# Kernel tuning notes

Measured on AMD Instinct MI355X. Metric: run time of the kernel, lower is better.

Reference implementation:

```python
import jax, jax.numpy as jnp
import numpy as np

B = 256      # batch size (molecules)
A = 64       # num_atoms per molecule
N = B * A    # total nodes = 16384
E = 262144   # num edges
H = 128      # hidden_dim
L = 4        # num_layers
LAT = 64     # latent_dim
AF = 16      # atom_feature_dim
LN_EPS = 1e-5


def setup_inputs() -> dict:
    key = jax.random.key(0)
    ks = jax.random.split(key, 26)
    w = lambda k, shape: (jax.random.normal(k, shape) * 0.05).astype(jnp.float32)
    inp = {}
    inp["z"] = jax.random.normal(ks[0], (B, LAT), jnp.float32)
    inp["atom_types"] = jax.nn.one_hot(
        jax.random.randint(ks[1], (N,), 0, AF), AF, dtype=jnp.float32)
    inp["pos0"] = jax.random.normal(ks[2], (N, 3), jnp.float32) * 0.1
    inp["edge_index"] = jax.random.randint(ks[3], (2, E), 0, N)
    # latent injector: Linear(LAT+AF, 2H) -> SiLU -> Linear(2H, H) -> SiLU -> Linear(H, H)
    inp["inj_W1"] = w(ks[4], (AF + LAT, 2 * H)); inp["inj_b1"] = jnp.zeros((2 * H,), jnp.float32)
    inp["inj_W2"] = w(ks[5], (2 * H, H));        inp["inj_b2"] = jnp.zeros((H,), jnp.float32)
    inp["inj_W3"] = w(ks[6], (H, H));            inp["inj_b3"] = jnp.zeros((H,), jnp.float32)
    # per-layer params, stacked over layer dim L
    inp["edge_W1"] = w(ks[7], (L, 2 * H + 1, H)); inp["edge_b1"] = jnp.zeros((L, H), jnp.float32)
    inp["edge_W2"] = w(ks[8], (L, H, H));         inp["edge_b2"] = jnp.zeros((L, H), jnp.float32)
    inp["coord_W1"] = w(ks[9], (L, H, H));        inp["coord_b1"] = jnp.zeros((L, H), jnp.float32)
    inp["coord_W2"] = w(ks[10], (L, H, 1))  # no bias
    inp["node_W1"] = w(ks[11], (L, 2 * H, H));    inp["node_b1"] = jnp.zeros((L, H), jnp.float32)
    inp["node_W2"] = w(ks[12], (L, H, H));        inp["node_b2"] = jnp.zeros((L, H), jnp.float32)
    inp["ln_g"] = jnp.ones((L, H), jnp.float32)
    inp["ln_b"] = jnp.zeros((L, H), jnp.float32)
    return inp


def _layer_norm(x, g, b):
    mu = jnp.mean(x, axis=-1, keepdims=True)
    var = jnp.mean((x - mu) ** 2, axis=-1, keepdims=True)
    return (x - mu) * jax.lax.rsqrt(var + LN_EPS) * g + b


def _egnn_layer(h, pos, row, col, eW1, eb1, eW2, eb2, cW1, cb1, cW2, nW1, nb1, nW2, nb2, g, b):
    # --- message: gather endpoints, edge MLP ---
    rel = pos[row] - pos[col]                                   # [E, 3]
    dsq = jnp.clip(jnp.sum(rel * rel, axis=1, keepdims=True), 1e-6, 1e6)  # [E, 1]
    ef = jnp.concatenate([h[row], h[col], dsq], axis=1)         # [E, 2H+1]
    m = jax.nn.silu(ef @ eW1 + eb1)
    m = jax.nn.silu(m @ eW2 + eb2)
    m = jnp.clip(m, -10.0, 10.0)                                # [E, H]
    # --- coordinate update: coord MLP -> weighted rel_pos -> scatter_add, mean-normalized ---
    cw = jax.nn.silu(m @ cW1 + cb1) @ cW2                       # [E, 1]
    coord_update = jax.ops.segment_sum(cw * rel, row, num_segments=N)   # [N, 3]
    num_neighbors = jax.ops.segment_sum(jnp.ones((row.shape[0],), m.dtype), row, num_segments=N)[:, None]
    pos_new = pos + coord_update / (num_neighbors + 1e-6)
    # --- node update: scatter_add messages, node MLP, residual + LayerNorm ---
    agg = jax.ops.segment_sum(m, row, num_segments=N)           # [N, H]
    nu = jnp.concatenate([h, agg], axis=1)                      # [N, 2H]
    nu = jax.nn.silu(nu @ nW1 + nb1) @ nW2 + nb2
    h_new = _layer_norm(h + nu, g, b)
    return h_new, pos_new


def reference(z, atom_types, pos0, edge_index,
              inj_W1, inj_b1, inj_W2, inj_b2, inj_W3, inj_b3,
              edge_W1, edge_b1, edge_W2, edge_b2,
              coord_W1, coord_b1, coord_W2,
              node_W1, node_b1, node_W2, node_b2,
              ln_g, ln_b):
    # latent injection: h = MLP(cat[atom_types, repeat_interleave(z, num_atoms)])
    z_exp = jnp.repeat(z, A, axis=0)                            # [N, LAT]
    h = jnp.concatenate([atom_types, z_exp], axis=1)            # [N, AF+LAT]
    h = jax.nn.silu(h @ inj_W1 + inj_b1)
    h = jax.nn.silu(h @ inj_W2 + inj_b2)
    h = h @ inj_W3 + inj_b3                                     # [N, H]
    pos = pos0
    row, col = edge_index[0], edge_index[1]
    for l in range(L):
        h, pos = _egnn_layer(h, pos, row, col,
                             edge_W1[l], edge_b1[l], edge_W2[l], edge_b2[l],
                             coord_W1[l], coord_b1[l], coord_W2[l],
                             node_W1[l], node_b1[l], node_W2[l], node_b2[l],
                             ln_g[l], ln_b[l])
    return pos
```

## Files before the change

### kernel.cpp

```cpp
#include <hip/hip_runtime.h>
#include <cmath>

#define N_NODES 16384
#define E_EDGES 262144
#define HD 128
#define NLAYER 4

typedef __attribute__((ext_vector_type(8))) short bf16x8;
typedef __attribute__((ext_vector_type(4))) float f32x4;
#define MFMA16(a, b, c) __builtin_amdgcn_mfma_f32_16x16x32_bf16(a, b, c, 0, 0, 0)

__device__ __forceinline__ float silu_f(float x) {
  return __fdividef(x, 1.0f + __expf(-x));
}

__device__ __forceinline__ unsigned short bf16_rn(float f) {
  union { float f; unsigned u; } v; v.f = f;
  unsigned r = (v.u + 0x7FFFu + ((v.u >> 16) & 1u)) >> 16;
  return (unsigned short)r;
}
__device__ __forceinline__ float bf16_tof(unsigned short h) {
  union { unsigned u; float f; } v; v.u = ((unsigned)h) << 16; return v.f;
}

__global__ void k_prep_w(const float* __restrict__ eW1, const float* __restrict__ eW2,
                         const float* __restrict__ cW1,
                         unsigned short* __restrict__ e1f, unsigned short* __restrict__ e2f,
                         unsigned short* __restrict__ c1f) {
  int sid = blockIdx.x * 256 + threadIdx.x;
  int layer = sid >> 13;
  int r = sid & 8191;
  const float* src; unsigned short* base; int c, s, halfstride;
  if (r < 4096) {
    c = r >> 9; s = r & 511;
    src = eW1 + (size_t)layer * 257 * 128;
    base = e1f + (size_t)layer * 65536; halfstride = 32768;
  } else if (r < 6144) {
    int rr = r - 4096; c = rr >> 9; s = rr & 511;
    src = eW2 + (size_t)layer * 128 * 128;
    base = e2f + (size_t)layer * 32768; halfstride = 16384;
  } else {
    int rr = r - 6144; c = rr >> 9; s = rr & 511;
    src = cW1 + (size_t)layer * 128 * 128;
    base = c1f + (size_t)layer * 32768; halfstride = 16384;
  }
  int cf = s >> 6, lp = s & 63;
  int n = cf * 16 + (lp & 15);
  int k0 = c * 32 + (lp >> 4) * 8;
  bf16x8 hv, lv;
#pragma unroll
  for (int j = 0; j < 8; ++j) {
    float w = src[(size_t)(k0 + j) * 128 + n];
    unsigned short h = bf16_rn(w);
    hv[j] = (short)h;
    lv[j] = (short)bf16_rn(w - bf16_tof(h));
  }
  size_t off = ((size_t)c * 512 + s) * 8;
  *(bf16x8*)(base + off) = hv;
  *(bf16x8*)(base + halfstride + off) = lv;
}

__global__ void k_h2bf(const float* __restrict__ h, unsigned short* __restrict__ hhi,
                       unsigned short* __restrict__ hlo) {
  int i = (blockIdx.x * 256 + threadIdx.x) * 8;
  float4 a = *(const float4*)(h + i), b = *(const float4*)(h + i + 4);
  float v[8] = {a.x, a.y, a.z, a.w, b.x, b.y, b.z, b.w};
  bf16x8 hv, lv;
#pragma unroll
  for (int j = 0; j < 8; ++j) {
    unsigned u = __float_as_uint(v[j]);
    hv[j] = (short)(u >> 16);
    float hi_f = __uint_as_float(u & 0xFFFF0000u);
    lv[j] = (short)bf16_rn(v[j] - hi_f);
  }
  *(bf16x8*)(hhi + i) = hv;
  *(bf16x8*)(hlo + i) = lv;
}

__global__ __launch_bounds__(256, 3) void k_edge_mfma(
    const unsigned short* __restrict__ hhi, const unsigned short* __restrict__ hlo,
    const float* __restrict__ pos,
    const int* __restrict__ rows, const int* __restrict__ cols, const int* __restrict__ perm,
    const unsigned short* __restrict__ e1f, const float* __restrict__ eW1,
    const float* __restrict__ eb1,
    const unsigned short* __restrict__ e2f, const float* __restrict__ eb2,
    const unsigned short* __restrict__ c1f, const float* __restrict__ cb1,
    const float* __restrict__ cW2,
    float* __restrict__ agg, float* __restrict__ coordacc) {
  __shared__ __align__(16) float T[64][132];
  __shared__ __align__(16) short Bl[2][4096];
  __shared__ int srow[64], scol[64];
  __shared__ float sdsq[64];
  __shared__ float srel[64][4];

  const int tid = threadIdx.x;
  const int lane = tid & 63;
  const int w = tid >> 6;
  const int l15 = lane & 15, l4 = lane >> 4;
  const int j0 = blockIdx.x * 64;
  const f32x4 zero4 = {0.f, 0.f, 0.f, 0.f};

  if (tid < 64) {
    int e = perm[j0 + tid];
    int r = rows[e], c = cols[e];
    srow[tid] = r; scol[tid] = c;
    float rx = pos[r * 3 + 0] - pos[c * 3 + 0];
    float ry = pos[r * 3 + 1] - pos[c * 3 + 1];
    float rz = pos[r * 3 + 2] - pos[c * 3 + 2];
    srel[tid][0] = rx; srel[tid][1] = ry; srel[tid][2] = rz;
    float d = rx * rx + ry * ry + rz * rz;
    sdsq[tid] = fminf(fmaxf(d, 1e-6f), 1e6f);
  }

  f32x4 acc[8];

#pragma unroll
  for (int i = 0; i < 8; ++i) acc[i] = zero4;
  for (int c = 0; c < 8; ++c) {
    __syncthreads();
#pragma unroll
    for (int t = 0; t < 4; ++t) {
      int slot = tid + t * 256;
      int half = slot >> 9, rem = slot & 511;
      const unsigned short* src = e1f + (size_t)half * 32768 + ((size_t)c * 512 + rem) * 8;
      *(bf16x8*)(&Bl[half][rem * 8]) = *(const bf16x8*)src;
    }
    __syncthreads();
    int node = (c < 4 ? srow : scol)[16 * w + l15];
    int koff = (c & 3) * 32 + l4 * 8;
    bf16x8 ah = *(const bf16x8*)(hhi + (size_t)node * 128 + koff);
    bf16x8 al = *(const bf16x8*)(hlo + (size_t)node * 128 + koff);
#pragma unroll
    for (int cf = 0; cf < 8; ++cf) {
      bf16x8 bh = *(const bf16x8*)(&Bl[0][cf * 512 + lane * 8]);
      bf16x8 bl = *(const bf16x8*)(&Bl[1][cf * 512 + lane * 8]);
      acc[cf] = MFMA16(ah, bh, acc[cf]);
      acc[cf] = MFMA16(al, bh, acc[cf]);
      acc[cf] = MFMA16(ah, bl, acc[cf]);
    }
  }
#pragma unroll
  for (int cf = 0; cf < 8; ++cf) {
    int col = cf * 16 + l15;
    float wl = eW1[256 * 128 + col];
    float bb = eb1[col];
#pragma unroll
    for (int r = 0; r < 4; ++r) {
      int trow = 16 * w + l4 * 4 + r;
      T[trow][col] = silu_f(acc[cf][r] + sdsq[trow] * wl + bb);
    }
  }

#pragma unroll
  for (int i = 0; i < 8; ++i) acc[i] = zero4;
  for (int c = 0; c < 4; ++c) {
    __syncthreads();
#pragma unroll
    for (int t = 0; t < 4; ++t) {
      int slot = tid + t * 256;
      int half = slot >> 9, rem = slot & 511;
      const unsigned short* src = e2f + (size_t)half * 16384 + ((size_t)c * 512 + rem) * 8;
      *(bf16x8*)(&Bl[half][rem * 8]) = *(const bf16x8*)src;
    }
    __syncthreads();
    int trow = 16 * w + l15;
    int k0 = c * 32 + l4 * 8;
    float tv[8];
    *(float4*)(tv) = *(const float4*)(&T[trow][k0]);
    *(float4*)(tv + 4) = *(const float4*)(&T[trow][k0 + 4]);
    bf16x8 ah, al;
#pragma unroll
    for (int j = 0; j < 8; ++j) {
      unsigned u = __float_as_uint(tv[j]);
      ah[j] = (short)(u >> 16);
      float hi_f = __uint_as_float(u & 0xFFFF0000u);
      al[j] = (short)bf16_rn(tv[j] - hi_f);
    }
#pragma unroll
    for (int cf = 0; cf < 8; ++cf) {
      bf16x8 bh = *(const bf16x8*)(&Bl[0][cf * 512 + lane * 8]);
      bf16x8 bl = *(const bf16x8*)(&Bl[1][cf * 512 + lane * 8]);
      acc[cf] = MFMA16(ah, bh, acc[cf]);
      acc[cf] = MFMA16(al, bh, acc[cf]);
      acc[cf] = MFMA16(ah, bl, acc[cf]);
    }
  }
#pragma unroll
  for (int cf = 0; cf < 8; ++cf) {
    int col = cf * 16 + l15;
    float bb = eb2[col];
#pragma unroll
    for (int r = 0; r < 4; ++r) {
      int trow = 16 * w + l4 * 4 + r;
      float v = silu_f(acc[cf][r] + bb);
      v = fminf(fmaxf(v, -10.0f), 10.0f);
      acc[cf][r] = v;
      T[trow][col] = v;
    }
  }
  {
    int seg = 0;
    while (seg < 16) {
      int node = srow[16 * w + seg];
      int se = seg + 1;
      while (se < 16 && srow[16 * w + se] == node) ++se;
#pragma unroll
      for (int cf = 0; cf < 8; ++cf) {
        float s = 0.f;
#pragma unroll
        for (int r = 0; r < 4; ++r) {
          int row = l4 * 4 + r;
          s += (row >= seg && row < se) ? acc[cf][r] : 0.f;
        }
        s += __shfl_xor(s, 16);
        s += __shfl_xor(s, 32);
        if (l4 == 0) atomicAdd(&agg[(size_t)node * 128 + cf * 16 + l15], s);
      }
      seg = se;
    }
  }

#pragma unroll
  for (int i = 0; i < 8; ++i) acc[i] = zero4;
  for (int c = 0; c < 4; ++c) {
    __syncthreads();
#pragma unroll
    for (int t = 0; t < 4; ++t) {
      int slot = tid + t * 256;
      int half = slot >> 9, rem = slot & 511;
      const unsigned short* src = c1f + (size_t)half * 16384 + ((size_t)c * 512 + rem) * 8;
      *(bf16x8*)(&Bl[half][rem * 8]) = *(const bf16x8*)src;
    }
    __syncthreads();
    int trow = 16 * w + l15;
    int k0 = c * 32 + l4 * 8;
    float tv[8];
    *(float4*)(tv) = *(const float4*)(&T[trow][k0]);
    *(float4*)(tv + 4) = *(const float4*)(&T[trow][k0 + 4]);
    bf16x8 ah, al;
#pragma unroll
    for (int j = 0; j < 8; ++j) {
      unsigned u = __float_as_uint(tv[j]);
      ah[j] = (short)(u >> 16);
      float hi_f = __uint_as_float(u & 0xFFFF0000u);
      al[j] = (short)bf16_rn(tv[j] - hi_f);
    }
#pragma unroll
    for (int cf = 0; cf < 8; ++cf) {
      bf16x8 bh = *(const bf16x8*)(&Bl[0][cf * 512 + lane * 8]);
      bf16x8 bl = *(const bf16x8*)(&Bl[1][cf * 512 + lane * 8]);
      acc[cf] = MFMA16(ah, bh, acc[cf]);
      acc[cf] = MFMA16(al, bh, acc[cf]);
      acc[cf] = MFMA16(ah, bl, acc[cf]);
    }
  }
  {
    float p[4] = {0.f, 0.f, 0.f, 0.f};
#pragma unroll
    for (int cf = 0; cf < 8; ++cf) {
      int col = cf * 16 + l15;
      float bb = cb1[col];
      float w2 = cW2[col];
#pragma unroll
      for (int r = 0; r < 4; ++r) p[r] += silu_f(acc[cf][r] + bb) * w2;
    }
#pragma unroll
    for (int d = 1; d < 16; d <<= 1) {
#pragma unroll
      for (int r = 0; r < 4; ++r) p[r] += __shfl_xor(p[r], d);
    }
    int seg = 0;
    while (seg < 16) {
      int node = srow[16 * w + seg];
      int se = seg + 1;
      while (se < 16 && srow[16 * w + se] == node) ++se;
      float s = 0.f;
      if (l15 < 3) {
#pragma unroll
        for (int r = 0; r < 4; ++r) {
          int row = l4 * 4 + r;
          s += (row >= seg && row < se) ? p[r] * srel[16 * w + row][l15] : 0.f;
        }
      }
      s += __shfl_xor(s, 16);
      s += __shfl_xor(s, 32);
      if (l4 == 0 && l15 < 3) atomicAdd(&coordacc[(size_t)node * 4 + l15], s);
      seg = se;
    }
  }
}

__global__ void k_pos_fin(const float* __restrict__ coordacc, const int* __restrict__ offs,
                          float* __restrict__ pos) {
  int n = blockIdx.x * 256 + threadIdx.x;
  if (n < N_NODES) {
    float deg = (float)(offs[n + 1] - offs[n]);
    float inv = __fdividef(1.0f, deg + 1e-6f);
    pos[n * 3 + 0] += coordacc[n * 4 + 0] * inv;
    pos[n * 3 + 1] += coordacc[n * 4 + 1] * inv;
    pos[n * 3 + 2] += coordacc[n * 4 + 2] * inv;
  }
}

template <int ACT>
__global__ __launch_bounds__(256, 2) void k_gemm128(const float* Ag, const float* __restrict__ W,
                                                    const float* __restrict__ bias, float* C, int K) {
  __shared__ float As[64][33];
  __shared__ float Ws[32][128];
  const int tid = threadIdx.x;
  const int tc = tid & 15, tr = tid >> 4;
  const int tr4 = tr * 4, tc4 = tc * 4;
  const int m0 = blockIdx.x * 64;

  float acc[4][8];
#pragma unroll
  for (int i = 0; i < 4; ++i)
#pragma unroll
    for (int j = 0; j < 8; ++j) acc[i][j] = 0.0f;

  for (int kk = 0; kk < K; kk += 32) {
    int idx = tid;
#pragma unroll
    for (int it = 0; it < 2; ++it, idx += 256) {
      int r = idx >> 3, c4 = (idx & 7) << 2;
      float4 v = *(const float4*)(Ag + (size_t)(m0 + r) * K + kk + c4);
      As[r][c4] = v.x; As[r][c4 + 1] = v.y; As[r][c4 + 2] = v.z; As[r][c4 + 3] = v.w;
    }
    idx = tid;
#pragma unroll
    for (int it = 0; it < 4; ++it, idx += 256) {
      int r = idx >> 5, c4 = (idx & 31) << 2;
      *(float4*)(&Ws[r][c4]) = *(const float4*)(W + (size_t)(kk + r) * 128 + c4);
    }
    __syncthreads();
#pragma unroll
    for (int k = 0; k < 32; ++k) {
      float av[4];
#pragma unroll
      for (int i = 0; i < 4; ++i) av[i] = As[tr4 + i][k];
      float4 b0 = *(const float4*)(&Ws[k][tc4]);
      float4 b1 = *(const float4*)(&Ws[k][64 + tc4]);
      float bv[8] = {b0.x, b0.y, b0.z, b0.w, b1.x, b1.y, b1.z, b1.w};
#pragma unroll
      for (int i = 0; i < 4; ++i)
#pragma unroll
        for (int j = 0; j < 8; ++j) acc[i][j] = fmaf(av[i], bv[j], acc[i][j]);
    }
    __syncthreads();
  }

  float bv0[8];
#pragma unroll
  for (int j = 0; j < 4; ++j) { bv0[j] = bias[tc4 + j]; bv0[4 + j] = bias[64 + tc4 + j]; }
#pragma unroll
  for (int i = 0; i < 4; ++i) {
    size_t row = m0 + tr4 + i;
    float o[8];
#pragma unroll
    for (int j = 0; j < 8; ++j) {
      float v = acc[i][j] + bv0[j];
      if (ACT >= 1) v = silu_f(v);
      o[j] = v;
    }
    *(float4*)(C + row * 128 + tc4) = make_float4(o[0], o[1], o[2], o[3]);
    *(float4*)(C + row * 128 + 64 + tc4) = make_float4(o[4], o[5], o[6], o[7]);
  }
}

__global__ void k_count(const int* __restrict__ rows, int* __restrict__ cnt) {
  int e = blockIdx.x * 256 + threadIdx.x;
  if (e < E_EDGES) atomicAdd(&cnt[rows[e]], 1);
}

__global__ void k_scan(const int* __restrict__ cnt, int* __restrict__ offs) {
  __shared__ int part[256];
  const int tid = threadIdx.x;
  const int base = tid * 64;
  int s = 0;
  for (int i = 0; i < 64; ++i) s += cnt[base + i];
  part[tid] = s;
  __syncthreads();
  for (int d = 1; d < 256; d <<= 1) {
    int v = (tid >= d) ? part[tid - d] : 0;
    __syncthreads();
    part[tid] += v;
    __syncthreads();
  }
  int run = part[tid] - s;
  for (int i = 0; i < 64; ++i) { offs[base + i] = run; run += cnt[base + i]; }
  if (tid == 255) offs[N_NODES] = run;
}

__global__ void k_fill(const int* __restrict__ rows, const int* __restrict__ offs,
                       int* __restrict__ fill, int* __restrict__ perm) {
  int e = blockIdx.x * 256 + threadIdx.x;
  if (e < E_EDGES) {
    int r = rows[e];
    int p = atomicAdd(&fill[r], 1);
    perm[offs[r] + p] = e;
  }
}

__global__ __launch_bounds__(256, 2) void k_node_mlp(float* __restrict__ h, const float* __restrict__ agg,
                                                     const float* __restrict__ W1, const float* __restrict__ b1,
                                                     const float* __restrict__ W2, const float* __restrict__ b2,
                                                     const float* __restrict__ lng, const float* __restrict__ lnb) {
  __shared__ float As[64][33];
  __shared__ float Ws[32][128];
  __shared__ float T[64][132];
  const int tid = threadIdx.x;
  const int tc = tid & 15, tr = tid >> 4;
  const int tr4 = tr * 4, tc4 = tc * 4;
  const int m0 = blockIdx.x * 64;

  float acc[4][8];
#pragma unroll
  for (int i = 0; i < 4; ++i)
#pragma unroll
    for (int j = 0; j < 8; ++j) acc[i][j] = 0.0f;

  for (int kk = 0; kk < 256; kk += 32) {
    const float* src = (kk < 128) ? h : agg;
    const int kb = kk & 127;
    int idx = tid;
#pragma unroll
    for (int it = 0; it < 2; ++it, idx += 256) {
      int r = idx >> 3, c4 = (idx & 7) << 2;
      float4 v = *(const float4*)(src + (size_t)(m0 + r) * 128 + kb + c4);
      As[r][c4] = v.x; As[r][c4 + 1] = v.y; As[r][c4 + 2] = v.z; As[r][c4 + 3] = v.w;
    }
    idx = tid;
#pragma unroll
    for (int it = 0; it < 4; ++it, idx += 256) {
      int r = idx >> 5, c4 = (idx & 31) << 2;
      *(float4*)(&Ws[r][c4]) = *(const float4*)(W1 + (size_t)(kk + r) * 128 + c4);
    }
    __syncthreads();
#pragma unroll
    for (int k = 0; k < 32; ++k) {
      float av[4];
#pragma unroll
      for (int i = 0; i < 4; ++i) av[i] = As[tr4 + i][k];
      float4 b0 = *(const float4*)(&Ws[k][tc4]);
      float4 b1v = *(const float4*)(&Ws[k][64 + tc4]);
      float bv[8] = {b0.x, b0.y, b0.z, b0.w, b1v.x, b1v.y, b1v.z, b1v.w};
#pragma unroll
      for (int i = 0; i < 4; ++i)
#pragma unroll
        for (int j = 0; j < 8; ++j) acc[i][j] = fmaf(av[i], bv[j], acc[i][j]);
    }
    __syncthreads();
  }
#pragma unroll
  for (int i = 0; i < 4; ++i) {
#pragma unroll
    for (int j = 0; j < 4; ++j) {
      T[tr4 + i][tc4 + j] = silu_f(acc[i][j] + b1[tc4 + j]);
      T[tr4 + i][64 + tc4 + j] = silu_f(acc[i][4 + j] + b1[64 + tc4 + j]);
    }
  }
  __syncthreads();

  float acc2[4][8];
#pragma unroll
  for (int i = 0; i < 4; ++i)
#pragma unroll
    for (int j = 0; j < 8; ++j) acc2[i][j] = 0.0f;
  for (int kk = 0; kk < 128; kk += 32) {
    int idx = tid;
#pragma unroll
    for (int it = 0; it < 4; ++it, idx += 256) {
      int r = idx >> 5, c4 = (idx & 31) << 2;
      *(float4*)(&Ws[r][c4]) = *(const float4*)(W2 + (size_t)(kk + r) * 128 + c4);
    }
    __syncthreads();
#pragma unroll
    for (int k = 0; k < 32; ++k) {
      float av[4];
#pragma unroll
      for (int i = 0; i < 4; ++i) av[i] = T[tr4 + i][kk + k];
      float4 b0 = *(const float4*)(&Ws[k][tc4]);
      float4 b1v = *(const float4*)(&Ws[k][64 + tc4]);
      float bv[8] = {b0.x, b0.y, b0.z, b0.w, b1v.x, b1v.y, b1v.z, b1v.w};
#pragma unroll
      for (int i = 0; i < 4; ++i)
#pragma unroll
        for (int j = 0; j < 8; ++j) acc2[i][j] = fmaf(av[i], bv[j], acc2[i][j]);
    }
    __syncthreads();
  }

  float x[4][8], s1[4], s2[4];
#pragma unroll
  for (int i = 0; i < 4; ++i) {
    size_t row = m0 + tr4 + i;
    float4 h0 = *(const float4*)(h + row * 128 + tc4);
    float4 h1 = *(const float4*)(h + row * 128 + 64 + tc4);
    float hv[8] = {h0.x, h0.y, h0.z, h0.w, h1.x, h1.y, h1.z, h1.w};
    s1[i] = 0.f; s2[i] = 0.f;
#pragma unroll
    for (int j = 0; j < 8; ++j) {
      int cidx = (j < 4) ? (tc4 + j) : (64 + tc4 + (j - 4));
      float v = hv[j] + acc2[i][j] + b2[cidx];
      x[i][j] = v;
      s1[i] += v;
      s2[i] += v * v;
    }
  }
#pragma unroll
  for (int d = 1; d < 16; d <<= 1) {
#pragma unroll
    for (int i = 0; i < 4; ++i) {
      s1[i] += __shfl_xor(s1[i], d);
      s2[i] += __shfl_xor(s2[i], d);
    }
  }
  float gv[8], bvv[8];
#pragma unroll
  for (int j = 0; j < 4; ++j) {
    gv[j] = lng[tc4 + j]; gv[4 + j] = lng[64 + tc4 + j];
    bvv[j] = lnb[tc4 + j]; bvv[4 + j] = lnb[64 + tc4 + j];
  }
#pragma unroll
  for (int i = 0; i < 4; ++i) {
    float mu = s1[i] * (1.0f / 128.0f);
    float var = s2[i] * (1.0f / 128.0f) - mu * mu;
    float rs = rsqrtf(var + 1e-5f);
    size_t row = m0 + tr4 + i;
    float o[8];
#pragma unroll
    for (int j = 0; j < 8; ++j) o[j] = (x[i][j] - mu) * rs * gv[j] + bvv[j];
    *(float4*)(h + row * 128 + tc4) = make_float4(o[0], o[1], o[2], o[3]);
    *(float4*)(h + row * 128 + 64 + tc4) = make_float4(o[4], o[5], o[6], o[7]);
  }
}

__global__ __launch_bounds__(256) void k_inj1(const float* __restrict__ at, const float* __restrict__ z,
                                              const float* __restrict__ W1, const float* __restrict__ b1,
                                              float* __restrict__ out) {
  __shared__ float As[64][84];
  __shared__ float Ws[80][128];
  const int tid = threadIdx.x;
  const int tc = tid & 15, tr = tid >> 4;
  const int tr4 = tr * 4, tc4 = tc * 4;
  const int m0 = blockIdx.y * 64;
  const int cb = blockIdx.x * 128;

  int idx = tid;
#pragma unroll
  for (int it = 0; it < 5; ++it, idx += 256) {
    int r = idx / 20, c4 = idx % 20;
    int n = m0 + r;
    float4 v;
    if (c4 < 4) v = *(const float4*)(at + (size_t)n * 16 + c4 * 4);
    else v = *(const float4*)(z + (size_t)(n >> 6) * 64 + (c4 - 4) * 4);
    *(float4*)(&As[r][c4 * 4]) = v;
  }
  idx = tid;
#pragma unroll
  for (int it = 0; it < 10; ++it, idx += 256) {
    int r = idx >> 5, c4 = (idx & 31) << 2;
    *(float4*)(&Ws[r][c4]) = *(const float4*)(W1 + (size_t)r * 256 + cb + c4);
  }
  __syncthreads();

  float acc[4][8];
#pragma unroll
  for (int i = 0; i < 4; ++i)
#pragma unroll
    for (int j = 0; j < 8; ++j) acc[i][j] = 0.0f;
#pragma unroll 4
  for (int k = 0; k < 80; ++k) {
    float av[4];
#pragma unroll
    for (int i = 0; i < 4; ++i) av[i] = As[tr4 + i][k];
    float4 b0 = *(const float4*)(&Ws[k][tc4]);
    float4 b1v = *(const float4*)(&Ws[k][64 + tc4]);
    float bv[8] = {b0.x, b0.y, b0.z, b0.w, b1v.x, b1v.y, b1v.z, b1v.w};
#pragma unroll
    for (int i = 0; i < 4; ++i)
#pragma unroll
      for (int j = 0; j < 8; ++j) acc[i][j] = fmaf(av[i], bv[j], acc[i][j]);
  }

  float bb[8];
#pragma unroll
  for (int j = 0; j < 4; ++j) { bb[j] = b1[cb + tc4 + j]; bb[4 + j] = b1[cb + 64 + tc4 + j]; }
#pragma unroll
  for (int i = 0; i < 4; ++i) {
    size_t row = m0 + tr4 + i;
    float o[8];
#pragma unroll
    for (int j = 0; j < 8; ++j) o[j] = silu_f(acc[i][j] + bb[j]);
    *(float4*)(out + row * 256 + cb + tc4) = make_float4(o[0], o[1], o[2], o[3]);
    *(float4*)(out + row * 256 + cb + 64 + tc4) = make_float4(o[4], o[5], o[6], o[7]);
  }
}

__global__ void k_copyf(const float* __restrict__ in, float* __restrict__ out, int n) {
  int i = blockIdx.x * 256 + threadIdx.x;
  if (i < n) out[i] = in[i];
}

extern "C" void kernel_launch(void* const* d_in, const int* in_sizes, int n_in,
                              void* d_out, int out_size, void* d_ws, size_t ws_size,
                              hipStream_t stream) {
  const float* z = (const float*)d_in[0];
  const float* at = (const float*)d_in[1];
  const float* pos0 = (const float*)d_in[2];
  const int* ei = (const int*)d_in[3];
  const float* injW1 = (const float*)d_in[4];
  const float* injb1 = (const float*)d_in[5];
  const float* injW2 = (const float*)d_in[6];
  const float* injb2 = (const float*)d_in[7];
  const float* injW3 = (const float*)d_in[8];
  const float* injb3 = (const float*)d_in[9];
  const float* eW1 = (const float*)d_in[10];
  const float* eb1 = (const float*)d_in[11];
  const float* eW2 = (const float*)d_in[12];
  const float* eb2 = (const float*)d_in[13];
  const float* cW1 = (const float*)d_in[14];
  const float* cb1 = (const float*)d_in[15];
  const float* cW2 = (const float*)d_in[16];
  const float* nW1 = (const float*)d_in[17];
  const float* nb1 = (const float*)d_in[18];
  const float* nW2 = (const float*)d_in[19];
  const float* nb2 = (const float*)d_in[20];
  const float* lng = (const float*)d_in[21];
  const float* lnb = (const float*)d_in[22];

  float* w = (float*)d_ws;
  float* h = w;        w += (size_t)N_NODES * HD;
  float* pos = w;      w += (size_t)N_NODES * 3;
  float* agg = w;      w += (size_t)N_NODES * HD;
  float* coordacc = w; w += (size_t)N_NODES * 4;
  float* t1 = w;       w += (size_t)N_NODES * 256;
  float* t2 = w;       w += (size_t)N_NODES * HD;
  unsigned short* hhi = (unsigned short*)w;
  unsigned short* hlo = hhi + (size_t)N_NODES * HD;
  unsigned short* e1f = hlo + (size_t)N_NODES * HD;
  unsigned short* e2f = e1f + (size_t)4 * 65536;
  unsigned short* c1f = e2f + (size_t)4 * 32768;
  int* ib = (int*)(c1f + (size_t)4 * 32768);
  int* cnt = ib;  ib += N_NODES;
  int* offs = ib; ib += N_NODES + 1;
  int* fill = ib; ib += N_NODES;
  int* perm = ib; ib += E_EDGES;

  const int* rowsp = ei;
  const int* colsp = ei + E_EDGES;

  hipMemsetAsync(cnt, 0, N_NODES * sizeof(int), stream);
  hipMemsetAsync(fill, 0, N_NODES * sizeof(int), stream);
  k_count<<<E_EDGES / 256, 256, 0, stream>>>(rowsp, cnt);
  k_scan<<<1, 256, 0, stream>>>(cnt, offs);
  k_fill<<<E_EDGES / 256, 256, 0, stream>>>(rowsp, offs, fill, perm);
  k_copyf<<<(N_NODES * 3 + 255) / 256, 256, 0, stream>>>(pos0, pos, N_NODES * 3);

  k_prep_w<<<128, 256, 0, stream>>>(eW1, eW2, cW1, e1f, e2f, c1f);

  k_inj1<<<dim3(2, N_NODES / 64), 256, 0, stream>>>(at, z, injW1, injb1, t1);
  k_gemm128<1><<<N_NODES / 64, 256, 0, stream>>>(t1, injW2, injb2, t2, 256);
  k_gemm128<0><<<N_NODES / 64, 256, 0, stream>>>(t2, injW3, injb3, h, 128);

  for (int l = 0; l < NLAYER; ++l) {
    hipMemsetAsync(agg, 0, (size_t)N_NODES * HD * sizeof(float), stream);
    hipMemsetAsync(coordacc, 0, (size_t)N_NODES * 4 * sizeof(float), stream);
    k_h2bf<<<(N_NODES * HD / 8) / 256, 256, 0, stream>>>(h, hhi, hlo);
    k_edge_mfma<<<E_EDGES / 64, 256, 0, stream>>>(
        hhi, hlo, pos, rowsp, colsp, perm,
        e1f + (size_t)l * 65536, eW1 + (size_t)l * 257 * HD, eb1 + l * HD,
        e2f + (size_t)l * 32768, eb2 + l * HD,
        c1f + (size_t)l * 32768, cb1 + l * HD,
        cW2 + (size_t)l * HD,
        agg, coordacc);
    k_pos_fin<<<N_NODES / 256, 256, 0, stream>>>(coordacc, offs, pos);
    k_node_mlp<<<N_NODES / 64, 256, 0, stream>>>(h, agg, nW1 + (size_t)l * 2 * HD * HD, nb1 + l * HD,
                                                 nW2 + (size_t)l * HD * HD, nb2 + l * HD,
                                                 lng + l * HD, lnb + l * HD);
  }
  k_copyf<<<(N_NODES * 3 + 255) / 256, 256, 0, stream>>>(pos, (float*)d_out, N_NODES * 3);
}
```

Measured before the change: 1.088 ms.

## Repartition edge MFMA warps by column tiles and store split-bf16 intermediates

```diff
diff --git a/kernel.cpp b/kernel.cpp
--- a/kernel.cpp
+++ b/kernel.cpp
@@ -87,7 +87,8 @@
     const unsigned short* __restrict__ c1f, const float* __restrict__ cb1,
     const float* __restrict__ cW2,
     float* __restrict__ agg, float* __restrict__ coordacc) {
-  __shared__ __align__(16) float T[64][132];
+  __shared__ __align__(16) unsigned short Thi[64][136];
+  __shared__ __align__(16) unsigned short Tlo[64][136];
   __shared__ __align__(16) short Bl[2][4096];
   __shared__ int srow[64], scol[64];
   __shared__ float sdsq[64];
@@ -112,10 +113,10 @@
     sdsq[tid] = fminf(fmaxf(d, 1e-6f), 1e6f);
   }
 
-  f32x4 acc[8];
-
-#pragma unroll
-  for (int i = 0; i < 8; ++i) acc[i] = zero4;
+  f32x4 acc[4][2];
+
+#pragma unroll
+  for (int rt = 0; rt < 4; ++rt) { acc[rt][0] = zero4; acc[rt][1] = zero4; }
   for (int c = 0; c < 8; ++c) {
     __syncthreads();
 #pragma unroll
@@ -126,33 +127,47 @@
       *(bf16x8*)(&Bl[half][rem * 8]) = *(const bf16x8*)src;
     }
     __syncthreads();
-    int node = (c < 4 ? srow : scol)[16 * w + l15];
+    bf16x8 bh[2], bl[2];
+#pragma unroll
+    for (int cfl = 0; cfl < 2; ++cfl) {
+      int cf = 2 * w + cfl;
+      bh[cfl] = *(const bf16x8*)(&Bl[0][cf * 512 + lane * 8]);
+      bl[cfl] = *(const bf16x8*)(&Bl[1][cf * 512 + lane * 8]);
+    }
+    const int* nodes = (c < 4) ? srow : scol;
     int koff = (c & 3) * 32 + l4 * 8;
-    bf16x8 ah = *(const bf16x8*)(hhi + (size_t)node * 128 + koff);
-    bf16x8 al = *(const bf16x8*)(hlo + (size_t)node * 128 + koff);
-#pragma unroll
-    for (int cf = 0; cf < 8; ++cf) {
-      bf16x8 bh = *(const bf16x8*)(&Bl[0][cf * 512 + lane * 8]);
-      bf16x8 bl = *(const bf16x8*)(&Bl[1][cf * 512 + lane * 8]);
-      acc[cf] = MFMA16(ah, bh, acc[cf]);
-      acc[cf] = MFMA16(al, bh, acc[cf]);
-      acc[cf] = MFMA16(ah, bl, acc[cf]);
-    }
-  }
-#pragma unroll
-  for (int cf = 0; cf < 8; ++cf) {
-    int col = cf * 16 + l15;
+#pragma unroll
+    for (int rt = 0; rt < 4; ++rt) {
+      int node = nodes[rt * 16 + l15];
+      bf16x8 ah = *(const bf16x8*)(hhi + (size_t)node * 128 + koff);
+      bf16x8 al = *(const bf16x8*)(hlo + (size_t)node * 128 + koff);
+#pragma unroll
+      for (int cfl = 0; cfl < 2; ++cfl) {
+        acc[rt][cfl] = MFMA16(ah, bh[cfl], acc[rt][cfl]);
+        acc[rt][cfl] = MFMA16(al, bh[cfl], acc[rt][cfl]);
+        acc[rt][cfl] = MFMA16(ah, bl[cfl], acc[rt][cfl]);
+      }
+    }
+  }
+#pragma unroll
+  for (int cfl = 0; cfl < 2; ++cfl) {
+    int col = (2 * w + cfl) * 16 + l15;
     float wl = eW1[256 * 128 + col];
     float bb = eb1[col];
 #pragma unroll
-    for (int r = 0; r < 4; ++r) {
-      int trow = 16 * w + l4 * 4 + r;
-      T[trow][col] = silu_f(acc[cf][r] + sdsq[trow] * wl + bb);
-    }
-  }
-
-#pragma unroll
-  for (int i = 0; i < 8; ++i) acc[i] = zero4;
+    for (int rt = 0; rt < 4; ++rt)
+#pragma unroll
+      for (int r = 0; r < 4; ++r) {
+        int trow = rt * 16 + l4 * 4 + r;
+        float v = silu_f(acc[rt][cfl][r] + sdsq[trow] * wl + bb);
+        unsigned u = __float_as_uint(v);
+        Thi[trow][col] = (unsigned short)(u >> 16);
+        Tlo[trow][col] = bf16_rn(v - __uint_as_float(u & 0xFFFF0000u));
+      }
+  }
+
+#pragma unroll
+  for (int rt = 0; rt < 4; ++rt) { acc[rt][0] = zero4; acc[rt][1] = zero4; }
   for (int c = 0; c < 4; ++c) {
     __syncthreads();
 #pragma unroll
@@ -163,65 +178,73 @@
       *(bf16x8*)(&Bl[half][rem * 8]) = *(const bf16x8*)src;
     }
     __syncthreads();
-    int trow = 16 * w + l15;
+    bf16x8 bh[2], bl[2];
+#pragma unroll
+    for (int cfl = 0; cfl < 2; ++cfl) {
+      int cf = 2 * w + cfl;
+      bh[cfl] = *(const bf16x8*)(&Bl[0][cf * 512 + lane * 8]);
+      bl[cfl] = *(const bf16x8*)(&Bl[1][cf * 512 + lane * 8]);
+    }
     int k0 = c * 32 + l4 * 8;
-    float tv[8];
-    *(float4*)(tv) = *(const float4*)(&T[trow][k0]);
-    *(float4*)(tv + 4) = *(const float4*)(&T[trow][k0 + 4]);
-    bf16x8 ah, al;
-#pragma unroll
-    for (int j = 0; j < 8; ++j) {
-      unsigned u = __float_as_uint(tv[j]);
-      ah[j] = (short)(u >> 16);
-      float hi_f = __uint_as_float(u & 0xFFFF0000u);
-      al[j] = (short)bf16_rn(tv[j] - hi_f);
-    }
-#pragma unroll
-    for (int cf = 0; cf < 8; ++cf) {
-      bf16x8 bh = *(const bf16x8*)(&Bl[0][cf * 512 + lane * 8]);
-      bf16x8 bl = *(const bf16x8*)(&Bl[1][cf * 512 + lane * 8]);
-      acc[cf] = MFMA16(ah, bh, acc[cf]);
-      acc[cf] = MFMA16(al, bh, acc[cf]);
-      acc[cf] = MFMA16(ah, bl, acc[cf]);
-    }
-  }
-#pragma unroll
-  for (int cf = 0; cf < 8; ++cf) {
-    int col = cf * 16 + l15;
+#pragma unroll
+    for (int rt = 0; rt < 4; ++rt) {
+      int trow = rt * 16 + l15;
+      bf16x8 ah = *(const bf16x8*)(&Thi[trow][k0]);
+      bf16x8 al = *(const bf16x8*)(&Tlo[trow][k0]);
+#pragma unroll
+      for (int cfl = 0; cfl < 2; ++cfl) {
+        acc[rt][cfl] = MFMA16(ah, bh[cfl], acc[rt][cfl]);
+        acc[rt][cfl] = MFMA16(al, bh[cfl], acc[rt][cfl]);
+        acc[rt][cfl] = MFMA16(ah, bl[cfl], acc[rt][cfl]);
+      }
+    }
+  }
+  __syncthreads();
+#pragma unroll
+  for (int cfl = 0; cfl < 2; ++cfl) {
+    int col = (2 * w + cfl) * 16 + l15;
     float bb = eb2[col];
 #pragma unroll
-    for (int r = 0; r < 4; ++r) {
-      int trow = 16 * w + l4 * 4 + r;
-      float v = silu_f(acc[cf][r] + bb);
-      v = fminf(fmaxf(v, -10.0f), 10.0f);
-      acc[cf][r] = v;
-      T[trow][col] = v;
-    }
+    for (int rt = 0; rt < 4; ++rt)
+#pragma unroll
+      for (int r = 0; r < 4; ++r) {
+        int trow = rt * 16 + l4 * 4 + r;
+        float v = silu_f(acc[rt][cfl][r] + bb);
+        v = fminf(fmaxf(v, -10.0f), 10.0f);
+        acc[rt][cfl][r] = v;
+        unsigned u = __float_as_uint(v);
+        Thi[trow][col] = (unsigned short)(u >> 16);
+        Tlo[trow][col] = bf16_rn(v - __uint_as_float(u & 0xFFFF0000u));
+      }
   }
   {
     int seg = 0;
-    while (seg < 16) {
-      int node = srow[16 * w + seg];
+    while (seg < 64) {
+      int node = srow[seg];
       int se = seg + 1;
-      while (se < 16 && srow[16 * w + se] == node) ++se;
-#pragma unroll
-      for (int cf = 0; cf < 8; ++cf) {
+      while (se < 64 && srow[se] == node) ++se;
+#pragma unroll
+      for (int cfl = 0; cfl < 2; ++cfl) {
         float s = 0.f;
 #pragma unroll
-        for (int r = 0; r < 4; ++r) {
-          int row = l4 * 4 + r;
-          s += (row >= seg && row < se) ? acc[cf][r] : 0.f;
+        for (int rt = 0; rt < 4; ++rt) {
+          if (rt * 16 + 15 < seg || rt * 16 >= se) continue;
+#pragma unroll
+          for (int r = 0; r < 4; ++r) {
+            int row = rt * 16 + l4 * 4 + r;
+            s += (row >= seg && row < se) ? acc[rt][cfl][r] : 0.f;
+          }
         }
         s += __shfl_xor(s, 16);
         s += __shfl_xor(s, 32);
-        if (l4 == 0) atomicAdd(&agg[(size_t)node * 128 + cf * 16 + l15], s);
+        if (l4 == 0) atomicAdd(&agg[(size_t)node * 128 + (2 * w + cfl) * 16 + l15], s);
       }
       seg = se;
     }
   }
 
 #pragma unroll
-  for (int i = 0; i < 8; ++i) acc[i] = zero4;
+  for (int rt = 0; rt < 4; ++rt) { acc[rt][0] = zero4; acc[rt][1] = zero4; }
   for (int c = 0; c < 4; ++c) {
     __syncthreads();
 #pragma unroll
@@ -232,54 +255,65 @@
       *(bf16x8*)(&Bl[half][rem * 8]) = *(const bf16x8*)src;
     }
     __syncthreads();
-    int trow = 16 * w + l15;
+    bf16x8 bh[2], bl[2];
+#pragma unroll
+    for (int cfl = 0; cfl < 2; ++cfl) {
+      int cf = 2 * w + cfl;
+      bh[cfl] = *(const bf16x8*)(&Bl[0][cf * 512 + lane * 8]);
+      bl[cfl] = *(const bf16x8*)(&Bl[1][cf * 512 + lane * 8]);
+    }
     int k0 = c * 32 + l4 * 8;
-    float tv[8];
-    *(float4*)(tv) = *(const float4*)(&T[trow][k0]);
-    *(float4*)(tv + 4) = *(const float4*)(&T[trow][k0 + 4]);
-    bf16x8 ah, al;
-#pragma unroll
-    for (int j = 0; j < 8; ++j) {
-      unsigned u = __float_as_uint(tv[j]);
-      ah[j] = (short)(u >> 16);
-      float hi_f = __uint_as_float(u & 0xFFFF0000u);
-      al[j] = (short)bf16_rn(tv[j] - hi_f);
-    }
-#pragma unroll
-    for (int cf = 0; cf < 8; ++cf) {
-      bf16x8 bh = *(const bf16x8*)(&Bl[0][cf * 512 + lane * 8]);
-      bf16x8 bl = *(const bf16x8*)(&Bl[1][cf * 512 + lane * 8]);
-      acc[cf] = MFMA16(ah, bh, acc[cf]);
-      acc[cf] = MFMA16(al, bh, acc[cf]);
-      acc[cf] = MFMA16(ah, bl, acc[cf]);
+#pragma unroll
+    for (int rt = 0; rt < 4; ++rt) {
+      int trow = rt * 16 + l15;
+      bf16x8 ah = *(const bf16x8*)(&Thi[trow][k0]);
+      bf16x8 al = *(const bf16x8*)(&Tlo[trow][k0]);
+#pragma unroll
+      for (int cfl = 0; cfl < 2; ++cfl) {
+        acc[rt][cfl] = MFMA16(ah, bh[cfl], acc[rt][cfl]);
+        acc[rt][cfl] = MFMA16(al, bh[cfl], acc[rt][cfl]);
+        acc[rt][cfl] = MFMA16(ah, bl[cfl], acc[rt][cfl]);
+      }
     }
   }
   {
-    float p[4] = {0.f, 0.f, 0.f, 0.f};
-#pragma unroll
-    for (int cf = 0; cf < 8; ++cf) {
-      int col = cf * 16 + l15;
+    float p[4][4];
+#pragma unroll
+    for (int rt = 0; rt < 4; ++rt)
+#pragma unroll
+      for (int r = 0; r < 4; ++r) p[rt][r] = 0.f;
+#pragma unroll
+    for (int cfl = 0; cfl < 2; ++cfl) {
+      int col = (2 * w + cfl) * 16 + l15;
       float bb = cb1[col];
       float w2 = cW2[col];
 #pragma unroll
-      for (int r = 0; r < 4; ++r) p[r] += silu_f(acc[cf][r] + bb) * w2;
+      for (int rt = 0; rt < 4; ++rt)
+#pragma unroll
+        for (int r = 0; r < 4; ++r) p[rt][r] += silu_f(acc[rt][cfl][r] + bb) * w2;
     }
 #pragma unroll
     for (int d = 1; d < 16; d <<= 1) {
 #pragma unroll
-      for (int r = 0; r < 4; ++r) p[r] += __shfl_xor(p[r], d);
+      for (int rt = 0; rt < 4; ++rt)
+#pragma unroll
+        for (int r = 0; r < 4; ++r) p[rt][r] += __shfl_xor(p[rt][r], d);
     }
     int seg = 0;
-    while (seg < 16) {
-      int node = srow[16 * w + seg];
+    while (seg < 64) {
+      int node = srow[seg];
       int se = seg + 1;
-      while (se < 16 && srow[16 * w + se] == node) ++se;
+      while (se < 64 && srow[se] == node) ++se;
       float s = 0.f;
       if (l15 < 3) {
 #pragma unroll
-        for (int r = 0; r < 4; ++r) {
-          int row = l4 * 4 + r;
-          s += (row >= seg && row < se) ? p[r] * srel[16 * w + row][l15] : 0.f;
+        for (int rt = 0; rt < 4; ++rt) {
+          if (rt * 16 + 15 < seg || rt * 16 >= se) continue;
+#pragma unroll
+          for (int r = 0; r < 4; ++r) {
+            int row = rt * 16 + l4 * 4 + r;
+            s += (row >= seg && row < se) ? p[rt][r] * srel[row][l15] : 0.f;
+          }
         }
       }
       s += __shfl_xor(s, 16);
@@ -404,7 +438,9 @@
 __global__ __launch_bounds__(256, 2) void k_node_mlp(float* __restrict__ h, const float* __restrict__ agg,
                                                      const float* __restrict__ W1, const float* __restrict__ b1,
                                                      const float* __restrict__ W2, const float* __restrict__ b2,
-                                                     const float* __restrict__ lng, const float* __restrict__ lnb) {
+                                                     const float* __restrict__ lng, const float* __restrict__ lnb,
+                                                     unsigned short* __restrict__ hhi,
+                                                     unsigned short* __restrict__ hlo) {
   __shared__ float As[64][33];
   __shared__ float Ws[32][128];
   __shared__ float T[64][132];
@@ -528,10 +564,24 @@
     float rs = rsqrtf(var + 1e-5f);
     size_t row = m0 + tr4 + i;
     float o[8];
-#pragma unroll
-    for (int j = 0; j < 8; ++j) o[j] = (x[i][j] - mu) * rs * gv[j] + bvv[j];
+    unsigned hv16[8], lv16[8];
+#pragma unroll
+    for (int j = 0; j < 8; ++j) {
+      o[j] = (x[i][j] - mu) * rs * gv[j] + bvv[j];
+      unsigned u = __float_as_uint(o[j]);
+      hv16[j] = u >> 16;
+      lv16[j] = bf16_rn(o[j] - __uint_as_float(u & 0xFFFF0000u));
+    }
     *(float4*)(h + row * 128 + tc4) = make_float4(o[0], o[1], o[2], o[3]);
     *(float4*)(h + row * 128 + 64 + tc4) = make_float4(o[4], o[5], o[6], o[7]);
+    *(uint2*)(hhi + row * 128 + tc4) =
+        make_uint2(hv16[0] | (hv16[1] << 16), hv16[2] | (hv16[3] << 16));
+    *(uint2*)(hhi + row * 128 + 64 + tc4) =
+        make_uint2(hv16[4] | (hv16[5] << 16), hv16[6] | (hv16[7] << 16));
+    *(uint2*)(hlo + row * 128 + tc4) =
+        make_uint2(lv16[0] | (lv16[1] << 16), lv16[2] | (lv16[3] << 16));
+    *(uint2*)(hlo + row * 128 + 64 + tc4) =
+        make_uint2(lv16[4] | (lv16[5] << 16), lv16[6] | (lv16[7] << 16));
   }
 }
 
@@ -662,11 +712,11 @@
   k_inj1<<<dim3(2, N_NODES / 64), 256, 0, stream>>>(at, z, injW1, injb1, t1);
   k_gemm128<1><<<N_NODES / 64, 256, 0, stream>>>(t1, injW2, injb2, t2, 256);
   k_gemm128<0><<<N_NODES / 64, 256, 0, stream>>>(t2, injW3, injb3, h, 128);
+  k_h2bf<<<(N_NODES * HD / 8) / 256, 256, 0, stream>>>(h, hhi, hlo);
 
   for (int l = 0; l < NLAYER; ++l) {
     hipMemsetAsync(agg, 0, (size_t)N_NODES * HD * sizeof(float), stream);
     hipMemsetAsync(coordacc, 0, (size_t)N_NODES * 4 * sizeof(float), stream);
-    k_h2bf<<<(N_NODES * HD / 8) / 256, 256, 0, stream>>>(h, hhi, hlo);
     k_edge_mfma<<<E_EDGES / 64, 256, 0, stream>>>(
         hhi, hlo, pos, rowsp, colsp, perm,
         e1f + (size_t)l * 65536, eW1 + (size_t)l * 257 * HD, eb1 + l * HD,
@@ -677,7 +727,7 @@
     k_pos_fin<<<N_NODES / 256, 256, 0, stream>>>(coordacc, offs, pos);
     k_node_mlp<<<N_NODES / 64, 256, 0, stream>>>(h, agg, nW1 + (size_t)l * 2 * HD * HD, nb1 + l * HD,
                                                  nW2 + (size_t)l * HD * HD, nb2 + l * HD,
-                                                 lng + l * HD, lnb + l * HD);
+                                                 lng + l * HD, lnb + l * HD, hhi, hlo);
   }
   k_copyf<<<(N_NODES * 3 + 255) / 256, 256, 0, stream>>>(pos, (float*)d_out, N_NODES * 3);
 }
```

Result: slower. 1.364 ms (+25.4%).

## Load MFMA weight fragments from global directly and fuse bf16 split into node MLP

Applied to the files above, without the earlier changes.

```diff
diff --git a/kernel.cpp b/kernel.cpp
--- a/kernel.cpp
+++ b/kernel.cpp
@@ -77,7 +77,7 @@
   *(bf16x8*)(hlo + i) = lv;
 }
 
-__global__ __launch_bounds__(256, 3) void k_edge_mfma(
+__global__ __launch_bounds__(256, 4) void k_edge_mfma(
     const unsigned short* __restrict__ hhi, const unsigned short* __restrict__ hlo,
     const float* __restrict__ pos,
     const int* __restrict__ rows, const int* __restrict__ cols, const int* __restrict__ perm,
@@ -88,7 +88,6 @@
     const float* __restrict__ cW2,
     float* __restrict__ agg, float* __restrict__ coordacc) {
   __shared__ __align__(16) float T[64][132];
-  __shared__ __align__(16) short Bl[2][4096];
   __shared__ int srow[64], scol[64];
   __shared__ float sdsq[64];
   __shared__ float srel[64][4];
@@ -111,29 +110,22 @@
     float d = rx * rx + ry * ry + rz * rz;
     sdsq[tid] = fminf(fmaxf(d, 1e-6f), 1e6f);
   }
+  __syncthreads();
 
   f32x4 acc[8];
 
 #pragma unroll
   for (int i = 0; i < 8; ++i) acc[i] = zero4;
   for (int c = 0; c < 8; ++c) {
-    __syncthreads();
-#pragma unroll
-    for (int t = 0; t < 4; ++t) {
-      int slot = tid + t * 256;
-      int half = slot >> 9, rem = slot & 511;
-      const unsigned short* src = e1f + (size_t)half * 32768 + ((size_t)c * 512 + rem) * 8;
-      *(bf16x8*)(&Bl[half][rem * 8]) = *(const bf16x8*)src;
-    }
-    __syncthreads();
     int node = (c < 4 ? srow : scol)[16 * w + l15];
     int koff = (c & 3) * 32 + l4 * 8;
     bf16x8 ah = *(const bf16x8*)(hhi + (size_t)node * 128 + koff);
     bf16x8 al = *(const bf16x8*)(hlo + (size_t)node * 128 + koff);
+    const unsigned short* b0 = e1f + (size_t)c * 4096 + (size_t)lane * 8;
 #pragma unroll
     for (int cf = 0; cf < 8; ++cf) {
-      bf16x8 bh = *(const bf16x8*)(&Bl[0][cf * 512 + lane * 8]);
-      bf16x8 bl = *(const bf16x8*)(&Bl[1][cf * 512 + lane * 8]);
+      bf16x8 bh = *(const bf16x8*)(b0 + cf * 512);
+      bf16x8 bl = *(const bf16x8*)(b0 + 32768 + cf * 512);
       acc[cf] = MFMA16(ah, bh, acc[cf]);
       acc[cf] = MFMA16(al, bh, acc[cf]);
       acc[cf] = MFMA16(ah, bl, acc[cf]);
@@ -154,15 +146,6 @@
 #pragma unroll
   for (int i = 0; i < 8; ++i) acc[i] = zero4;
   for (int c = 0; c < 4; ++c) {
-    __syncthreads();
-#pragma unroll
-    for (int t = 0; t < 4; ++t) {
-      int slot = tid + t * 256;
-      int half = slot >> 9, rem = slot & 511;
-      const unsigned short* src = e2f + (size_t)half * 16384 + ((size_t)c * 512 + rem) * 8;
-      *(bf16x8*)(&Bl[half][rem * 8]) = *(const bf16x8*)src;
-    }
-    __syncthreads();
     int trow = 16 * w + l15;
     int k0 = c * 32 + l4 * 8;
     float tv[8];
@@ -176,10 +159,11 @@
       float hi_f = __uint_as_float(u & 0xFFFF0000u);
       al[j] = (short)bf16_rn(tv[j] - hi_f);
     }
+    const unsigned short* b0 = e2f + (size_t)c * 4096 + (size_t)lane * 8;
 #pragma unroll
     for (int cf = 0; cf < 8; ++cf) {
-      bf16x8 bh = *(const bf16x8*)(&Bl[0][cf * 512 + lane * 8]);
-      bf16x8 bl = *(const bf16x8*)(&Bl[1][cf * 512 + lane * 8]);
+      bf16x8 bh = *(const bf16x8*)(b0 + cf * 512);
+      bf16x8 bl = *(const bf16x8*)(b0 + 16384 + cf * 512);
       acc[cf] = MFMA16(ah, bh, acc[cf]);
       acc[cf] = MFMA16(al, bh, acc[cf]);
       acc[cf] = MFMA16(ah, bl, acc[cf]);
@@ -223,15 +207,6 @@
 #pragma unroll
   for (int i = 0; i < 8; ++i) acc[i] = zero4;
   for (int c = 0; c < 4; ++c) {
-    __syncthreads();
-#pragma unroll
-    for (int t = 0; t < 4; ++t) {
-      int slot = tid + t * 256;
-      int half = slot >> 9, rem = slot & 511;
-      const unsigned short* src = c1f + (size_t)half * 16384 + ((size_t)c * 512 + rem) * 8;
-      *(bf16x8*)(&Bl[half][rem * 8]) = *(const bf16x8*)src;
-    }
-    __syncthreads();
     int trow = 16 * w + l15;
     int k0 = c * 32 + l4 * 8;
     float tv[8];
@@ -245,10 +220,11 @@
       float hi_f = __uint_as_float(u & 0xFFFF0000u);
       al[j] = (short)bf16_rn(tv[j] - hi_f);
     }
+    const unsigned short* b0 = c1f + (size_t)c * 4096 + (size_t)lane * 8;
 #pragma unroll
     for (int cf = 0; cf < 8; ++cf) {
-      bf16x8 bh = *(const bf16x8*)(&Bl[0][cf * 512 + lane * 8]);
-      bf16x8 bl = *(const bf16x8*)(&Bl[1][cf * 512 + lane * 8]);
+      bf16x8 bh = *(const bf16x8*)(b0 + cf * 512);
+      bf16x8 bl = *(const bf16x8*)(b0 + 16384 + cf * 512);
       acc[cf] = MFMA16(ah, bh, acc[cf]);
       acc[cf] = MFMA16(al, bh, acc[cf]);
       acc[cf] = MFMA16(ah, bl, acc[cf]);
@@ -404,7 +380,9 @@
 __global__ __launch_bounds__(256, 2) void k_node_mlp(float* __restrict__ h, const float* __restrict__ agg,
                                                      const float* __restrict__ W1, const float* __restrict__ b1,
                                                      const float* __restrict__ W2, const float* __restrict__ b2,
-                                                     const float* __restrict__ lng, const float* __restrict__ lnb) {
+                                                     const float* __restrict__ lng, const float* __restrict__ lnb,
+                                                     unsigned short* __restrict__ hhi,
+                                                     unsigned short* __restrict__ hlo) {
   __shared__ float As[64][33];
   __shared__ float Ws[32][128];
   __shared__ float T[64][132];
@@ -528,10 +506,24 @@
     float rs = rsqrtf(var + 1e-5f);
     size_t row = m0 + tr4 + i;
     float o[8];
-#pragma unroll
-    for (int j = 0; j < 8; ++j) o[j] = (x[i][j] - mu) * rs * gv[j] + bvv[j];
+    unsigned hv16[8], lv16[8];
+#pragma unroll
+    for (int j = 0; j < 8; ++j) {
+      o[j] = (x[i][j] - mu) * rs * gv[j] + bvv[j];
+      unsigned u = __float_as_uint(o[j]);
+      hv16[j] = u >> 16;
+      lv16[j] = bf16_rn(o[j] - __uint_as_float(u & 0xFFFF0000u));
+    }
     *(float4*)(h + row * 128 + tc4) = make_float4(o[0], o[1], o[2], o[3]);
     *(float4*)(h + row * 128 + 64 + tc4) = make_float4(o[4], o[5], o[6], o[7]);
+    *(uint2*)(hhi + row * 128 + tc4) =
+        make_uint2(hv16[0] | (hv16[1] << 16), hv16[2] | (hv16[3] << 16));
+    *(uint2*)(hhi + row * 128 + 64 + tc4) =
+        make_uint2(hv16[4] | (hv16[5] << 16), hv16[6] | (hv16[7] << 16));
+    *(uint2*)(hlo + row * 128 + tc4) =
+        make_uint2(lv16[0] | (lv16[1] << 16), lv16[2] | (lv16[3] << 16));
+    *(uint2*)(hlo + row * 128 + 64 + tc4) =
+        make_uint2(lv16[4] | (lv16[5] << 16), lv16[6] | (lv16[7] << 16));
   }
 }
 
@@ -662,11 +654,11 @@
   k_inj1<<<dim3(2, N_NODES / 64), 256, 0, stream>>>(at, z, injW1, injb1, t1);
   k_gemm128<1><<<N_NODES / 64, 256, 0, stream>>>(t1, injW2, injb2, t2, 256);
   k_gemm128<0><<<N_NODES / 64, 256, 0, stream>>>(t2, injW3, injb3, h, 128);
+  k_h2bf<<<(N_NODES * HD / 8) / 256, 256, 0, stream>>>(h, hhi, hlo);
 
   for (int l = 0; l < NLAYER; ++l) {
     hipMemsetAsync(agg, 0, (size_t)N_NODES * HD * sizeof(float), stream);
     hipMemsetAsync(coordacc, 0, (size_t)N_NODES * 4 * sizeof(float), stream);
-    k_h2bf<<<(N_NODES * HD / 8) / 256, 256, 0, stream>>>(h, hhi, hlo);
     k_edge_mfma<<<E_EDGES / 64, 256, 0, stream>>>(
         hhi, hlo, pos, rowsp, colsp, perm,
         e1f + (size_t)l * 65536, eW1 + (size_t)l * 257 * HD, eb1 + l * HD,
@@ -677,7 +669,7 @@
     k_pos_fin<<<N_NODES / 256, 256, 0, stream>>>(coordacc, offs, pos);
     k_node_mlp<<<N_NODES / 64, 256, 0, stream>>>(h, agg, nW1 + (size_t)l * 2 * HD * HD, nb1 + l * HD,
                                                  nW2 + (size_t)l * HD * HD, nb2 + l * HD,
-                                                 lng + l * HD, lnb + l * HD);
+                                                 lng + l * HD, lnb + l * HD, hhi, hlo);
   }
   k_copyf<<<(N_NODES * 3 + 255) / 256, 256, 0, stream>>>(pos, (float*)d_out, N_NODES * 3);
 }
```

Result: slower. 1.190 ms (+9.4%).
